# Kernel optimization log

Hardware: AMD Instinct MI355X
Metric: run time of the kernel (lower is better)

Reference implementation:

```python
import jax, jax.numpy as jnp
import numpy as np

N_HEADS = 16

def setup_inputs() -> dict:
    key = jax.random.key(0)
    ks = jax.random.split(key, 6)
    B, H, F, P, D = 2048, 1024, 4096, 512, 1024
    x = jax.random.normal(ks[0], (B, H), dtype=jnp.float32)
    # module inits features/prototypes ~ U(-0.27, 1)
    features = jax.random.uniform(ks[1], (F, D), minval=-0.27, maxval=1.0, dtype=jnp.float32)
    prototypes = jax.random.uniform(ks[2], (P, D), minval=-0.27, maxval=1.0, dtype=jnp.float32)
    # theta/alpha/beta are zero-init in the module; use small random values so output is non-trivial
    theta = jax.random.normal(ks[3], (N_HEADS, 1), dtype=jnp.float32)
    alpha = jax.random.normal(ks[4], (N_HEADS, 1), dtype=jnp.float32)
    beta = jax.random.normal(ks[5], (N_HEADS, 1), dtype=jnp.float32)
    return {"x": x, "features": features, "prototypes": prototypes,
            "theta": theta, "alpha": alpha, "beta": beta}

def reference(x, features, prototypes, theta, alpha, beta):
    n_heads = N_HEADS
    B, total_dim = x.shape
    d = total_dim // n_heads
    xh = x.reshape(B, n_heads, d)                       # b h d
    fh = features.reshape(-1, n_heads, d).transpose(1, 0, 2)    # h f d
    ph = prototypes.reshape(-1, n_heads, d).transpose(1, 0, 2)  # h p d
    x_features = jnp.einsum('bhd,hfd->bhf', xh, fh)     # [B,h,F]
    p_features = jnp.einsum('hpd,hfd->hpf', ph, fh)     # [h,P,F]
    x_present = jax.nn.relu(x_features)
    p_present = jax.nn.relu(p_features)
    x_weighted = x_features * x_present
    p_weighted = p_features * p_present
    # head-batched GEMMs sharing operands
    common = jnp.einsum('bhf,hpf->bhp', x_weighted, p_weighted)
    x_p_interaction = jnp.einsum('bhf,hpf->bhp', x_weighted, p_present)
    p_x_interaction = jnp.einsum('bhf,hpf->bhp', x_present, p_weighted)
    x_weighted_sum = x_weighted.sum(axis=2, keepdims=True)      # [B,h,1]
    p_weighted_sum = p_weighted.sum(axis=2)[None, :, :]         # [1,h,P]
    x_distinctive = x_weighted_sum - x_p_interaction
    p_distinctive = p_weighted_sum - p_x_interaction
    th = theta.reshape(1, n_heads, 1)
    al = alpha.reshape(1, n_heads, 1)
    be = beta.reshape(1, n_heads, 1)
    out = th * common - al * x_distinctive - be * p_distinctive  # [B,h,P]
    return out.reshape(B, -1)
```

## Files before the change

### kernel.cpp

```cpp
#include <hip/hip_runtime.h>
#include <cstdint>

#define NH 16
#define DH 64
#define FF 4096
#define PP 512
#define BB 2048

typedef __bf16 bf16x8 __attribute__((ext_vector_type(8)));
typedef float f32x4 __attribute__((ext_vector_type(4)));
typedef float fl4 __attribute__((ext_vector_type(4)));
typedef unsigned short us4 __attribute__((ext_vector_type(4)));
typedef unsigned int u32x2 __attribute__((ext_vector_type(2)));

__device__ __forceinline__ unsigned short f2bf(float f) {
  unsigned u = __float_as_uint(f);
  u += 0x7FFFu + ((u >> 16) & 1u);
  return (unsigned short)(u >> 16);
}

__device__ __forceinline__ unsigned int pkbf(float lo, float hi) {
  unsigned a = __float_as_uint(lo) + 0x8000u;
  unsigned b = __float_as_uint(hi) + 0x8000u;
  return __builtin_amdgcn_perm(b, a, 0x07060302u);
}

__device__ __forceinline__ void gload_lds16(const void* g, void* l) {
  __builtin_amdgcn_global_load_lds(
      (const __attribute__((address_space(1))) void*)g,
      (__attribute__((address_space(3))) void*)(unsigned int)(unsigned long long)l,
      16, 0, 0);
}

__global__ void cvt_fp(const float* __restrict__ f, const float* __restrict__ p,
                       unsigned short* __restrict__ fb,
                       unsigned short* __restrict__ pb) {
  const int nf = FF * 1024 / 4, np = PP * 1024 / 4;
  int i = blockIdx.x * blockDim.x + threadIdx.x;
  const fl4* src;
  us4* dst;
  if (i < nf) {
    src = (const fl4*)f + i;
    dst = (us4*)fb + i;
  } else if (i < nf + np) {
    src = (const fl4*)p + (i - nf);
    dst = (us4*)pb + (i - nf);
  } else {
    return;
  }
  fl4 v = *src;
  us4 o;
  o.x = f2bf(v.x); o.y = f2bf(v.y); o.z = f2bf(v.z); o.w = f2bf(v.w);
  *dst = o;
}

__global__ __launch_bounds__(256, 2) void gemm_proto(
    const unsigned short* __restrict__ Abf, const unsigned short* __restrict__ Fbf,
    unsigned short* __restrict__ O1, unsigned short* __restrict__ O2,
    float* __restrict__ pws,
    const float* __restrict__ theta, const float* __restrict__ alpha,
    const float* __restrict__ beta) {
  const int h = blockIdx.z;
  const int n0 = blockIdx.x * 128;
  const int lm0 = blockIdx.y * 128;
  const int t = threadIdx.x;

  __shared__ __align__(16) char As[128 * 128];
  __shared__ __align__(16) char Bs[128 * 128];

  {
    const char* ab = (const char*)(Abf + (size_t)lm0 * 1024 + h * 64);
    const char* bb = (const char*)(Fbf + (size_t)n0 * 1024 + h * 64);
#pragma unroll
    for (int r = 0; r < 4; ++r) {
      int o = r * 4096 + t * 16;
      int row = o >> 7, col = o & 127;
      gload_lds16(ab + (size_t)row * 2048 + col, As + o);
      gload_lds16(bb + (size_t)row * 2048 + col, Bs + o);
    }
  }
  __syncthreads();

  const int wave = t >> 6, lane = t & 63;
  const int wm = wave & 1, wn = wave >> 1;
  const int quad = lane >> 4, lr = lane & 15;

  f32x4 acc[4][4];
#pragma unroll
  for (int i = 0; i < 4; ++i)
#pragma unroll
    for (int j = 0; j < 4; ++j) acc[i][j] = (f32x4){0.f, 0.f, 0.f, 0.f};

#pragma unroll
  for (int s = 0; s < 2; ++s) {
    bf16x8 av[4], bv[4];
#pragma unroll
    for (int fm = 0; fm < 4; ++fm) {
      int row = wm * 64 + fm * 16 + lr;
      av[fm] = *(const bf16x8*)(As + row * 128 + s * 64 + quad * 16);
    }
#pragma unroll
    for (int fn = 0; fn < 4; ++fn) {
      int row = wn * 64 + fn * 16 + lr;
      bv[fn] = *(const bf16x8*)(Bs + row * 128 + s * 64 + quad * 16);
    }
#pragma unroll
    for (int fm = 0; fm < 4; ++fm)
#pragma unroll
      for (int fn = 0; fn < 4; ++fn)
        acc[fm][fn] = __builtin_amdgcn_mfma_f32_16x16x32_bf16(av[fm], bv[fn],
                                                              acc[fm][fn], 0, 0, 0);
  }

  const float th = theta[h], al = alpha[h], be = beta[h];

#pragma unroll
  for (int fm = 0; fm < 4; ++fm) {
    int prow = lm0 + wm * 64 + fm * 16 + quad * 4;
    float rs0 = 0.f, rs1 = 0.f, rs2 = 0.f, rs3 = 0.f;
#pragma unroll
    for (int fn = 0; fn < 4; ++fn) {
      int f = n0 + wn * 64 + fn * 16 + lr;
#pragma unroll
      for (int i = 0; i < 4; ++i) {
        float pf = acc[fm][fn][i];
        float pp = fmaxf(pf, 0.f);
        float pw = pf * pp;
        size_t idx = ((size_t)(h * PP + prow + i)) * FF + f;
        O1[idx] = f2bf(th * pw + al * pp - al);
        O2[idx] = f2bf(be * pw);
        if (i == 0) rs0 += pw;
        else if (i == 1) rs1 += pw;
        else if (i == 2) rs2 += pw;
        else rs3 += pw;
      }
    }
    float rs[4] = {rs0, rs1, rs2, rs3};
#pragma unroll
    for (int i = 0; i < 4; ++i) {
      float s = rs[i];
      s += __shfl_xor(s, 1);
      s += __shfl_xor(s, 2);
      s += __shfl_xor(s, 4);
      s += __shfl_xor(s, 8);
      if (lr == 0) atomicAdd(&pws[h * PP + prow + i], be * s);
    }
  }
}

__global__ __launch_bounds__(256, 2) void fused_main(
    const float* __restrict__ x, const unsigned short* __restrict__ f_bf,
    const unsigned short* __restrict__ Q1, const unsigned short* __restrict__ Q2,
    const float* __restrict__ pws, float* __restrict__ out) {
  const int l = blockIdx.x;
  const int i = l >> 3;
  const int g = (l & 7) * 4 + (i & 3);
  const int h = g >> 1;
  const int n0 = (g & 1) * 256;
  const int m0 = (i >> 2) * 128;
  const int t = threadIdx.x;
  const int wave = t >> 6, lane = t & 63;
  const int quad = lane >> 4, lr = lane & 15;
  const int key8 = lr & 7;
  const int key2 = (lr >> 1) & 3;

  __shared__ __align__(16) char sF[2 * 4096];
  __shared__ __align__(16) char sXw[2 * 8192];
  __shared__ __align__(16) char sXp[2 * 8192];

  bf16x8 xh[2][2];
#pragma unroll
  for (int bn = 0; bn < 2; ++bn)
#pragma unroll
    for (int s = 0; s < 2; ++s) {
      int b = m0 + wave * 32 + bn * 16 + lr;
      const float* xr = x + (size_t)b * 1024 + h * 64 + s * 32 + quad * 8;
      fl4 v0 = *(const fl4*)xr;
      fl4 v1 = *(const fl4*)(xr + 4);
      union { unsigned u[4]; bf16x8 v; } cv;
      cv.u[0] = pkbf(v0.x, v0.y);
      cv.u[1] = pkbf(v0.z, v0.w);
      cv.u[2] = pkbf(v1.x, v1.y);
      cv.u[3] = pkbf(v1.z, v1.w);
      xh[bn][s] = cv.v;
    }

  int af_off[2][2];
#pragma unroll
  for (int fm = 0; fm < 2; ++fm)
#pragma unroll
    for (int s = 0; s < 2; ++s)
      af_off[fm][s] = (fm * 16 + lr) * 128 + (((s * 4 + quad) ^ key8) * 16);

  int cw_off[2][2];
#pragma unroll
  for (int fm = 0; fm < 2; ++fm)
#pragma unroll
    for (int bn = 0; bn < 2; ++bn)
      cw_off[fm][bn] = (wave * 32 + bn * 16 + lr) * 64 +
                       (((fm * 2 + (quad >> 1)) ^ key2) * 16) + (quad & 1) * 8;

  int aw_off[8];
#pragma unroll
  for (int fm = 0; fm < 8; ++fm)
    aw_off[fm] = (fm * 16 + lr) * 64 + ((quad ^ key2) * 16);

  const char* srcF;
  {
    int row = t >> 3, c = t & 7, cs = c ^ (row & 7);
    srcF = (const char*)f_bf + h * 128 + (size_t)row * 2048 + cs * 16;
  }

  const unsigned short* qrow1 =
      Q1 + (size_t)(h * PP + n0 + wave * 64 + lr) * FF + quad * 8;
  const unsigned short* qrow2 =
      Q2 + (size_t)(h * PP + n0 + wave * 64 + lr) * FF + quad * 8;

  f32x4 acc[8][4];
#pragma unroll
  for (int i2 = 0; i2 < 8; ++i2)
#pragma unroll
    for (int j = 0; j < 4; ++j) acc[i2][j] = (f32x4){0.f, 0.f, 0.f, 0.f};

  auto runBC = [&](int sfb, int xb) {
    f32x4 xf[2][2];
#pragma unroll
    for (int fm = 0; fm < 2; ++fm)
#pragma unroll
      for (int bn = 0; bn < 2; ++bn) xf[fm][bn] = (f32x4){0.f, 0.f, 0.f, 0.f};
#pragma unroll
    for (int s = 0; s < 2; ++s)
#pragma unroll
      for (int fm = 0; fm < 2; ++fm) {
        bf16x8 af = *(const bf16x8*)(sF + sfb + af_off[fm][s]);
#pragma unroll
        for (int bn = 0; bn < 2; ++bn)
          xf[fm][bn] = __builtin_amdgcn_mfma_f32_16x16x32_bf16(af, xh[bn][s],
                                                               xf[fm][bn], 0, 0, 0);
      }
#pragma unroll
    for (int fm = 0; fm < 2; ++fm)
#pragma unroll
      for (int bn = 0; bn < 2; ++bn) {
        float v0 = xf[fm][bn][0], v1 = xf[fm][bn][1];
        float v2 = xf[fm][bn][2], v3 = xf[fm][bn][3];
        float p0 = fmaxf(v0, 0.f), p1 = fmaxf(v1, 0.f);
        float p2 = fmaxf(v2, 0.f), p3 = fmaxf(v3, 0.f);
        u32x2 w, p;
        w.x = pkbf(v0 * p0, v1 * p1);
        w.y = pkbf(v2 * p2, v3 * p3);
        p.x = pkbf(p0, p1);
        p.y = pkbf(p2, p3);
        *(u32x2*)(sXw + xb + cw_off[fm][bn]) = w;
        *(u32x2*)(sXp + xb + cw_off[fm][bn]) = p;
      }
  };

  gload_lds16(srcF, sF + t * 16);
  srcF += 32 * 2048;
  asm volatile("s_waitcnt vmcnt(0)\n\ts_barrier" ::: "memory");
  __builtin_amdgcn_sched_barrier(0);
  gload_lds16(srcF, sF + 4096 + t * 16);
  srcF += 32 * 2048;
  runBC(0, 0);
  asm volatile("s_waitcnt vmcnt(0) lgkmcnt(0)\n\ts_barrier" ::: "memory");
  __builtin_amdgcn_sched_barrier(0);

  for (int it = 0; it < FF / 32; ++it) {
    const int pA = it & 1;
    const int pB = pA ^ 1;

    bf16x8 q1v[4], q2v[4];
#pragma unroll
    for (int fn = 0; fn < 4; ++fn) {
      q1v[fn] = *(const bf16x8*)(qrow1 + fn * (16 * FF));
      q2v[fn] = *(const bf16x8*)(qrow2 + fn * (16 * FF));
    }
    qrow1 += 32;
    qrow2 += 32;

    gload_lds16(srcF, sF + pA * 4096 + t * 16);
    srcF += 32 * 2048;

    runBC(pB * 4096, pB * 8192);

    __builtin_amdgcn_s_setprio(1);
#pragma unroll
    for (int hf = 0; hf < 2; ++hf) {
      bf16x8 aw[4], ap[4];
#pragma unroll
      for (int fm = 0; fm < 4; ++fm) {
        aw[fm] = *(const bf16x8*)(sXw + pA * 8192 + aw_off[hf * 4 + fm]);
        ap[fm] = *(const bf16x8*)(sXp + pA * 8192 + aw_off[hf * 4 + fm]);
      }
#pragma unroll
      for (int fn = 0; fn < 4; ++fn)
#pragma unroll
        for (int fm = 0; fm < 4; ++fm) {
          acc[hf * 4 + fm][fn] = __builtin_amdgcn_mfma_f32_16x16x32_bf16(
              aw[fm], q1v[fn], acc[hf * 4 + fm][fn], 0, 0, 0);
          acc[hf * 4 + fm][fn] = __builtin_amdgcn_mfma_f32_16x16x32_bf16(
              ap[fm], q2v[fn], acc[hf * 4 + fm][fn], 0, 0, 0);
        }
    }
    __builtin_amdgcn_s_setprio(0);

    asm volatile("s_waitcnt vmcnt(0) lgkmcnt(0)\n\ts_barrier" ::: "memory");
    __builtin_amdgcn_sched_barrier(0);
  }

#pragma unroll
  for (int fn = 0; fn < 4; ++fn) {
    int p = n0 + wave * 64 + fn * 16 + lr;
    float sub = pws[h * PP + p];
#pragma unroll
    for (int fm = 0; fm < 8; ++fm) {
      int brow = m0 + fm * 16 + quad * 4;
#pragma unroll
      for (int i2 = 0; i2 < 4; ++i2) {
        out[(size_t)(brow + i2) * (NH * PP) + h * PP + p] = acc[fm][fn][i2] - sub;
      }
    }
  }
}

extern "C" void kernel_launch(void* const* d_in, const int* in_sizes, int n_in,
                              void* d_out, int out_size, void* d_ws, size_t ws_size,
                              hipStream_t stream) {
  const float* x = (const float*)d_in[0];
  const float* features = (const float*)d_in[1];
  const float* prototypes = (const float*)d_in[2];
  const float* theta = (const float*)d_in[3];
  const float* alpha = (const float*)d_in[4];
  const float* beta = (const float*)d_in[5];
  float* out = (float*)d_out;

  char* ws = (char*)d_ws;
  size_t off = 0;
  auto carve = [&](size_t bytes) -> char* {
    char* p = ws + off;
    off += (bytes + 255) & ~(size_t)255;
    return p;
  };
  unsigned short* f_bf = (unsigned short*)carve((size_t)(FF + 64) * 1024 * 2);
  unsigned short* p_bf = (unsigned short*)carve((size_t)PP * 1024 * 2);
  unsigned short* Q1 = (unsigned short*)carve((size_t)NH * PP * FF * 2);
  unsigned short* Q2 = (unsigned short*)carve((size_t)NH * PP * FF * 2);
  float* pws = (float*)carve((size_t)NH * PP * 4);

  const int ncvt = (FF + PP) * 1024 / 4;
  cvt_fp<<<(ncvt + 255) / 256, 256, 0, stream>>>(features, prototypes, f_bf, p_bf);
  hipMemsetAsync(pws, 0, (size_t)NH * PP * 4, stream);

  gemm_proto<<<dim3(FF / 128, PP / 128, NH), 256, 0, stream>>>(
      p_bf, f_bf, Q1, Q2, pws, theta, alpha, beta);

  fused_main<<<dim3(512, 1, 1), 256, 0, stream>>>(
      x, f_bf, Q1, Q2, pws, out);
}
```

Baseline: 386.2 us.

## Interleave relu/pack epilogue with main MFMA chunks and use byte-offset Q addressing

Splits the per-iteration B-step (the x·features MFMAs plus the relu/weight/bf16 pack and LDS stores) so that the VALU packing work is spread across four chunks of the main GEMM MFMAs, with sched_barriers fencing each chunk. It also issues the LDS reads for the second half of the A fragments earlier. The aim is to hide VALU and LDS latency behind matrix-core work instead of serializing it. Q loads now use a base pointer plus an unsigned byte offset, which may let the compiler fold constant offsets into the load instructions. Risks are higher register pressure and scheduler constraints imposed by the barriers.

New measurement: 383.0 us. Within noise of the previous version (-0.8%).

```diff
diff --git a/kernel.cpp b/kernel.cpp
--- a/kernel.cpp
+++ b/kernel.cpp
@@ -211,10 +211,9 @@
     srcF = (const char*)f_bf + h * 128 + (size_t)row * 2048 + cs * 16;
   }
 
-  const unsigned short* qrow1 =
-      Q1 + (size_t)(h * PP + n0 + wave * 64 + lr) * FF + quad * 8;
-  const unsigned short* qrow2 =
-      Q2 + (size_t)(h * PP + n0 + wave * 64 + lr) * FF + quad * 8;
+  const char* qb1 = (const char*)Q1 + (size_t)(h * PP + n0) * FF * 2;
+  const char* qb2 = (const char*)Q2 + (size_t)(h * PP + n0) * FF * 2;
+  unsigned qo = (unsigned)(((wave * 64 + lr) * FF + quad * 8) * 2);
 
   f32x4 acc[8][4];
 #pragma unroll
@@ -222,39 +221,53 @@
 #pragma unroll
     for (int j = 0; j < 4; ++j) acc[i2][j] = (f32x4){0.f, 0.f, 0.f, 0.f};
 
-  auto runBC = [&](int sfb, int xb) {
-    f32x4 xf[2][2];
-#pragma unroll
-    for (int fm = 0; fm < 2; ++fm)
-#pragma unroll
-      for (int bn = 0; bn < 2; ++bn) xf[fm][bn] = (f32x4){0.f, 0.f, 0.f, 0.f};
-#pragma unroll
-    for (int s = 0; s < 2; ++s)
-#pragma unroll
-      for (int fm = 0; fm < 2; ++fm) {
-        bf16x8 af = *(const bf16x8*)(sF + sfb + af_off[fm][s]);
-#pragma unroll
-        for (int bn = 0; bn < 2; ++bn)
-          xf[fm][bn] = __builtin_amdgcn_mfma_f32_16x16x32_bf16(af, xh[bn][s],
-                                                               xf[fm][bn], 0, 0, 0);
-      }
-#pragma unroll
-    for (int fm = 0; fm < 2; ++fm)
-#pragma unroll
-      for (int bn = 0; bn < 2; ++bn) {
-        float v0 = xf[fm][bn][0], v1 = xf[fm][bn][1];
-        float v2 = xf[fm][bn][2], v3 = xf[fm][bn][3];
-        float p0 = fmaxf(v0, 0.f), p1 = fmaxf(v1, 0.f);
-        float p2 = fmaxf(v2, 0.f), p3 = fmaxf(v3, 0.f);
-        u32x2 w, p;
-        w.x = pkbf(v0 * p0, v1 * p1);
-        w.y = pkbf(v2 * p2, v3 * p3);
-        p.x = pkbf(p0, p1);
-        p.y = pkbf(p2, p3);
-        *(u32x2*)(sXw + xb + cw_off[fm][bn]) = w;
-        *(u32x2*)(sXp + xb + cw_off[fm][bn]) = p;
-      }
-  };
+  f32x4 xf[2][2];
+
+#define BSTEP(SFB) do {                                                      \
+    _Pragma("unroll") for (int fm_ = 0; fm_ < 2; ++fm_)                      \
+      _Pragma("unroll") for (int bn_ = 0; bn_ < 2; ++bn_)                    \
+        xf[fm_][bn_] = (f32x4){0.f, 0.f, 0.f, 0.f};                          \
+    _Pragma("unroll") for (int s_ = 0; s_ < 2; ++s_)                         \
+      _Pragma("unroll") for (int fm_ = 0; fm_ < 2; ++fm_) {                  \
+        bf16x8 af_ = *(const bf16x8*)(sF + (SFB) + af_off[fm_][s_]);         \
+        _Pragma("unroll") for (int bn_ = 0; bn_ < 2; ++bn_)                  \
+          xf[fm_][bn_] = __builtin_amdgcn_mfma_f32_16x16x32_bf16(            \
+              af_, xh[bn_][s_], xf[fm_][bn_], 0, 0, 0);                      \
+      }                                                                      \
+  } while (0)
+
+#define CPACK(FM, BN, XB) do {                                               \
+    float v0_ = xf[FM][BN][0], v1_ = xf[FM][BN][1];                          \
+    float v2_ = xf[FM][BN][2], v3_ = xf[FM][BN][3];                          \
+    float p0_ = fmaxf(v0_, 0.f), p1_ = fmaxf(v1_, 0.f);                      \
+    float p2_ = fmaxf(v2_, 0.f), p3_ = fmaxf(v3_, 0.f);                      \
+    u32x2 w_, p_;                                                            \
+    w_.x = pkbf(v0_ * p0_, v1_ * p1_);                                       \
+    w_.y = pkbf(v2_ * p2_, v3_ * p3_);                                       \
+    p_.x = pkbf(p0_, p1_);                                                   \
+    p_.y = pkbf(p2_, p3_);                                                   \
+    *(u32x2*)(sXw + (XB) + cw_off[FM][BN]) = w_;                             \
+    *(u32x2*)(sXp + (XB) + cw_off[FM][BN]) = p_;                             \
+  } while (0)
+
+#define DREAD(HF, XA) do {                                                   \
+    _Pragma("unroll") for (int fm_ = 0; fm_ < 4; ++fm_) {                    \
+      aw[fm_] = *(const bf16x8*)(sXw + (XA) + aw_off[(HF) * 4 + fm_]);       \
+      ap[fm_] = *(const bf16x8*)(sXp + (XA) + aw_off[(HF) * 4 + fm_]);       \
+    }                                                                        \
+  } while (0)
+
+#define DMFMA(HF, FNP) do {                                                  \
+    _Pragma("unroll") for (int f2_ = 0; f2_ < 2; ++f2_) {                    \
+      const int fn_ = (FNP) * 2 + f2_;                                       \
+      _Pragma("unroll") for (int fm_ = 0; fm_ < 4; ++fm_) {                  \
+        acc[(HF) * 4 + fm_][fn_] = __builtin_amdgcn_mfma_f32_16x16x32_bf16(  \
+            aw[fm_], q1v[fn_], acc[(HF) * 4 + fm_][fn_], 0, 0, 0);           \
+        acc[(HF) * 4 + fm_][fn_] = __builtin_amdgcn_mfma_f32_16x16x32_bf16(  \
+            ap[fm_], q2v[fn_], acc[(HF) * 4 + fm_][fn_], 0, 0, 0);           \
+      }                                                                      \
+    }                                                                        \
+  } while (0)
 
   gload_lds16(srcF, sF + t * 16);
   srcF += 32 * 2048;
@@ -262,47 +275,48 @@
   __builtin_amdgcn_sched_barrier(0);
   gload_lds16(srcF, sF + 4096 + t * 16);
   srcF += 32 * 2048;
-  runBC(0, 0);
+  BSTEP(0);
+  CPACK(0, 0, 0);
+  CPACK(0, 1, 0);
+  CPACK(1, 0, 0);
+  CPACK(1, 1, 0);
   asm volatile("s_waitcnt vmcnt(0) lgkmcnt(0)\n\ts_barrier" ::: "memory");
   __builtin_amdgcn_sched_barrier(0);
 
   for (int it = 0; it < FF / 32; ++it) {
     const int pA = it & 1;
     const int pB = pA ^ 1;
+    const int xa = pA * 8192, xb = pB * 8192;
 
     bf16x8 q1v[4], q2v[4];
 #pragma unroll
     for (int fn = 0; fn < 4; ++fn) {
-      q1v[fn] = *(const bf16x8*)(qrow1 + fn * (16 * FF));
-      q2v[fn] = *(const bf16x8*)(qrow2 + fn * (16 * FF));
-    }
-    qrow1 += 32;
-    qrow2 += 32;
+      q1v[fn] = *(const bf16x8*)(qb1 + qo + fn * 131072);
+      q2v[fn] = *(const bf16x8*)(qb2 + qo + fn * 131072);
+    }
+    qo += 64;
 
     gload_lds16(srcF, sF + pA * 4096 + t * 16);
     srcF += 32 * 2048;
 
-    runBC(pB * 4096, pB * 8192);
+    BSTEP(pB * 4096);
+    bf16x8 aw[4], ap[4];
+    DREAD(0, xa);
+    __builtin_amdgcn_sched_barrier(0);
 
     __builtin_amdgcn_s_setprio(1);
-#pragma unroll
-    for (int hf = 0; hf < 2; ++hf) {
-      bf16x8 aw[4], ap[4];
-#pragma unroll
-      for (int fm = 0; fm < 4; ++fm) {
-        aw[fm] = *(const bf16x8*)(sXw + pA * 8192 + aw_off[hf * 4 + fm]);
-        ap[fm] = *(const bf16x8*)(sXp + pA * 8192 + aw_off[hf * 4 + fm]);
-      }
-#pragma unroll
-      for (int fn = 0; fn < 4; ++fn)
-#pragma unroll
-        for (int fm = 0; fm < 4; ++fm) {
-          acc[hf * 4 + fm][fn] = __builtin_amdgcn_mfma_f32_16x16x32_bf16(
-              aw[fm], q1v[fn], acc[hf * 4 + fm][fn], 0, 0, 0);
-          acc[hf * 4 + fm][fn] = __builtin_amdgcn_mfma_f32_16x16x32_bf16(
-              ap[fm], q2v[fn], acc[hf * 4 + fm][fn], 0, 0, 0);
-        }
-    }
+    CPACK(0, 0, xb);
+    DMFMA(0, 0);
+    __builtin_amdgcn_sched_barrier(0);
+    CPACK(0, 1, xb);
+    DMFMA(0, 1);
+    DREAD(1, xa);
+    __builtin_amdgcn_sched_barrier(0);
+    CPACK(1, 0, xb);
+    DMFMA(1, 0);
+    __builtin_amdgcn_sched_barrier(0);
+    CPACK(1, 1, xb);
+    DMFMA(1, 1);
     __builtin_amdgcn_s_setprio(0);
 
     asm volatile("s_waitcnt vmcnt(0) lgkmcnt(0)\n\ts_barrier" ::: "memory");
```
